# Kernel optimization log

Hardware: AMD Instinct MI355X
Metric: run time of the kernel (lower is better)

The kernel has to match this reference:

```python
import jax, jax.numpy as jnp
import numpy as np

# ---- constants baked into the module (buffers / init defaults) ----
SAMPLE_RATE = 44100
K = 1.0 / SAMPLE_RATE                    # time step
MAX_OM = 10000.0 * 2.0 * np.pi           # fmax * 2*pi
MIN_OM = 20.0 * 2.0 * np.pi
LX = 0.5
TAU0, TAU1 = 6.0, 1.0
LOSS_F1 = 500.0
_OM2 = 2.0 * np.pi * LOSS_F1
_DOMSQ = _OM2 ** 2                        # OmDamp1 = 0
ALPHA = np.float32(3.0 * np.log(10.0) / _DOMSQ * (_OM2 ** 2 / TAU0))
BETA = np.float32(3.0 * np.log(10.0) / _DOMSQ * (1.0 / TAU1 - 1.0 / TAU0))
M_MAX = N_MAX = 80
_gm, _gn = np.meshgrid(np.arange(1, M_MAX + 1), np.arange(1, N_MAX + 1), indexing='ij')
M_VEC = jnp.asarray(_gm.reshape(-1), dtype=jnp.float32)   # [6400]
N_VEC = jnp.asarray(_gn.reshape(-1), dtype=jnp.float32)   # [6400]


def setup_inputs() -> dict:
    z = jnp.zeros((), dtype=jnp.float32)
    return {
        'mu_raw': z, 'D_over_mu_raw': z, 'T0_over_mu_raw': z,
        'Ly_raw': z, 'xo_raw': z, 'yo_raw': z,
        'num_samples': 44100,  # duration=1.0 s
    }


def reference(mu_raw, D_over_mu_raw, T0_over_mu_raw, Ly_raw, xo_raw, yo_raw, num_samples):
    sp = jax.nn.softplus
    mu = sp(mu_raw) + 1e-4
    D_over_mu = sp(D_over_mu_raw) + 1e-4
    T0_over_mu = sp(T0_over_mu_raw) + 1e-4
    Ly = 1.1 + (4.0 - 1.1) * ((jnp.tanh(Ly_raw) + 1.0) / 2.0)
    xo = 0.49 * LX + (1.0 - 0.49) * LX * ((jnp.tanh(xo_raw) + 1.0) / 2.0)
    yo = 0.51 * Ly + (1.0 - 0.51) * Ly * ((jnp.tanh(yo_raw) + 1.0) / 2.0)
    xi = 0.1 * LX
    yi = 0.1 * Ly

    pi = np.float32(np.pi)
    g1 = (M_VEC * pi / LX) ** 2 + (N_VEC * pi / Ly) ** 2          # [6400]
    omega = jnp.sqrt(jax.nn.relu(T0_over_mu * g1 + D_over_mu * g1 * g1))
    valid = ((omega <= MAX_OM) & (omega >= MIN_OM)).astype(omega.dtype)

    in_w = jnp.cos(xi * pi * M_VEC / LX) * jnp.cos(yi * pi * N_VEC / Ly)
    out_w = jnp.cos(xo * pi * M_VEC / LX) * jnp.cos(yo * pi * N_VEC / Ly)
    sigma = ALPHA + BETA * omega ** 2
    ms = 0.25 * mu * LX * Ly
    P = out_w * in_w * (K ** 2) * jnp.exp(-sigma * K) / ms * valid  # [6400]

    n = jnp.arange(num_samples, dtype=jnp.float32)                # [N]
    # [6400, N] damped-sinusoid matrix, then reduce over modes
    decay_env = jnp.exp(-sigma[:, None] * (n[None, :] - 1.0) * K)
    sine = jnp.sin(n[None, :] * (omega[:, None] * K)) / (jnp.sin(omega * K) + 1e-8)[:, None]
    displacement = jnp.sum(P[:, None] * decay_env * sine, axis=0)  # [N]

    # normalize=True, velCalc=False (module defaults)
    peak = jnp.max(jnp.abs(displacement)) + 1e-8
    return displacement / peak
```

## Files before the change

### kernel.cpp

```cpp
#include <hip/hip_runtime.h>
#include <math.h>

#define BLK 256
#define G 32
#define NMODES 6400
#define STRIPE (NMODES / G)
#define MDIM 80
#define TILE 1024
#define SPT 4

__device__ float4   g_rec1[NMODES];
__device__ float4   g_rec2[NMODES];
__device__ unsigned g_maxbits;

__device__ __forceinline__ float v_fract(float x){ float r; asm("v_fract_f32 %0, %1" : "=v"(r) : "v"(x)); return r; }
__device__ __forceinline__ float v_sin_rev(float x){ float r; asm("v_sin_f32 %0, %1" : "=v"(r) : "v"(x)); return r; }
__device__ __forceinline__ float v_cos_rev(float x){ float r; asm("v_cos_f32 %0, %1" : "=v"(r) : "v"(x)); return r; }
__device__ __forceinline__ float v_exp2(float x){ float r; asm("v_exp_f32 %0, %1" : "=v"(r) : "v"(x)); return r; }

__device__ __forceinline__ double softplus_d(double x) {
    return (x > 30.0) ? x : log1p(exp(x));
}

__global__ __launch_bounds__(BLK) void setup_kernel(
    const float* __restrict__ mu_raw_p, const float* __restrict__ Dmu_raw_p,
    const float* __restrict__ T0mu_raw_p, const float* __restrict__ Ly_raw_p,
    const float* __restrict__ xo_raw_p, const float* __restrict__ yo_raw_p)
{
    const int gid = blockIdx.x * BLK + threadIdx.x;
    if (gid == 0) g_maxbits = 0u;
    if (gid >= NMODES) return;

    const double PI_D     = 3.14159265358979323846;
    const double TWO_PI_D = 6.28318530717958647693;
    const double INV2PI_D = 0.15915494309189533577;
    const double LOG2E_D  = 1.44269504088896340736;
    const double LX = 0.5;
    const double Kd = 1.0 / 44100.0;
    const double MAX_OM = 10000.0 * TWO_PI_D;
    const double MIN_OM = 20.0 * TWO_PI_D;

    const double OM2   = TWO_PI_D * 500.0;
    const double DOMSQ = OM2 * OM2;
    const float ALPHA_F = (float)(3.0 * log(10.0) / DOMSQ * (OM2 * OM2 / 6.0));
    const float BETA_F  = (float)(3.0 * log(10.0) / DOMSQ * (1.0 / 1.0 - 1.0 / 6.0));

    const double mu   = softplus_d((double)mu_raw_p[0])  + 1e-4;
    const double Dmu  = softplus_d((double)Dmu_raw_p[0]) + 1e-4;
    const double T0mu = softplus_d((double)T0mu_raw_p[0]) + 1e-4;
    const double Ly   = 1.1 + (4.0 - 1.1) * ((tanh((double)Ly_raw_p[0]) + 1.0) * 0.5);
    const double xo   = 0.49 * LX + (1.0 - 0.49) * LX * ((tanh((double)xo_raw_p[0]) + 1.0) * 0.5);
    const double yo   = 0.51 * Ly + (1.0 - 0.51) * Ly * ((tanh((double)yo_raw_p[0]) + 1.0) * 0.5);
    const double xi = 0.1 * LX;
    const double yi = 0.1 * Ly;
    const double ms = 0.25 * mu * LX * Ly;

    const double mm = (double)(gid / MDIM + 1);
    const double nn = (double)(gid % MDIM + 1);
    const double a1 = mm * PI_D / LX;
    const double a2 = nn * PI_D / Ly;
    const double g1 = a1 * a1 + a2 * a2;
    double osq = T0mu * g1 + Dmu * g1 * g1;
    if (osq < 0.0) osq = 0.0;
    const double omega = sqrt(osq);

    float4 r1 = make_float4(0.0f, 0.0f, 0.0f, 0.0f);
    float4 r2 = make_float4(1.0f, 0.0f, 1.0f, 0.0f);
    if (omega >= MIN_OM && omega <= MAX_OM) {
        const double w     = omega * Kd;
        const double sig   = (double)ALPHA_F + (double)BETA_F * (omega * omega);
        const double in_w  = cos(xi * a1) * cos(yi * a2);
        const double out_w = cos(xo * a1) * cos(yo * a2);
        const double denom = sin(w) + 1e-8;
        const double A = out_w * in_w * (Kd * Kd) / ms / denom;
        const double wrev = w * INV2PI_D;
        const float hi = (float)wrev;
        const float lo = (float)(wrev - (double)hi);
        const double z = -sig * Kd * LOG2E_D;
        const double dph = 256.0 * w;
        r1 = make_float4(hi, lo, (float)z, (float)A);
        r2 = make_float4((float)cos(dph), (float)sin(dph),
                         (float)exp2(256.0 * z), 0.0f);
    }
    g_rec1[gid] = r1;
    g_rec2[gid] = r2;
}

__global__ __launch_bounds__(BLK) void modal_main_kernel(
    float* __restrict__ partial, int pstride)
{
    __shared__ float4 md1[STRIPE];
    __shared__ float4 md2[STRIPE];
    __shared__ int cnt;
    if (threadIdx.x == 0) cnt = 0;
    __syncthreads();

    const int n0  = blockIdx.x * TILE;
    const int gy  = blockIdx.y;
    const float n0f = (float)n0;
    const int lane = threadIdx.x & 63;

    {
        const int j = threadIdx.x;
        bool alive = false;
        float4 o1, o2;
        if (j < STRIPE) {
            const float4 rec = g_rec1[gy + G * j];
            if (rec.w != 0.0f) {
                const float amp0 = rec.w * v_exp2(rec.z * n0f);
                if (fabsf(amp0) >= 1e-20f) {
                    const double wrev = (double)rec.x + (double)rec.y;
                    const double p0   = (double)n0 * wrev;
                    const float base  = (float)(p0 - rint(p0));
                    o1 = make_float4(base, rec.x, rec.z, amp0);
                    o2 = g_rec2[gy + G * j];
                    alive = true;
                }
            }
        }
        const unsigned long long mask = __ballot(alive);
        const int nw = __popcll(mask);
        int base_slot = 0;
        if (lane == 0 && nw) base_slot = atomicAdd(&cnt, nw);
        base_slot = __shfl(base_slot, 0, 64);
        if (alive) {
            const int s = base_slot + __popcll(mask & ((1ull << lane) - 1ull));
            md1[s] = o1;
            md2[s] = o2;
        }
    }
    __syncthreads();

    const int count = cnt;
    const float tf = (float)threadIdx.x;
    float acc0 = 0.0f, acc1 = 0.0f, acc2 = 0.0f, acc3 = 0.0f;
    for (int j = 0; j < count; ++j) {
        const float4 v1 = md1[j];
        const float4 v2 = md2[j];
        const float rev = v_fract(fmaf(tf, v1.y, v1.x));
        float s = v_sin_rev(rev);
        float c = v_cos_rev(rev);
        float amp = v1.w * v_exp2(v1.z * tf);
        acc0 = fmaf(amp, s, acc0);
        const float cD = v2.x, sD = v2.y, eD = v2.z;
        float s1 = fmaf(s, cD,  c * sD);
        float c1 = fmaf(c, cD, -s * sD);
        amp *= eD;
        acc1 = fmaf(amp, s1, acc1);
        float s2 = fmaf(s1, cD,  c1 * sD);
        float c2 = fmaf(c1, cD, -s1 * sD);
        amp *= eD;
        acc2 = fmaf(amp, s2, acc2);
        float s3 = fmaf(s2, cD,  c2 * sD);
        amp *= eD;
        acc3 = fmaf(amp, s3, acc3);
        (void)c2; (void)s3;
    }
    float* row = partial + (size_t)gy * pstride + n0 + threadIdx.x;
    row[0]   = acc0;
    row[256] = acc1;
    row[512] = acc2;
    row[768] = acc3;
}

__global__ __launch_bounds__(BLK) void combine_max_kernel(
    const float* __restrict__ partial, int pstride,
    float* __restrict__ out, int N)
{
    const int nvec = N >> 2;
    const int i = blockIdx.x * BLK + threadIdx.x;
    float m = 0.0f;
    if (i < nvec) {
        float4 s = make_float4(0.0f, 0.0f, 0.0f, 0.0f);
        const float4* p4 = (const float4*)partial;
        const int vstride = pstride >> 2;
        #pragma unroll
        for (int g = 0; g < G; ++g) {
            const float4 v = p4[(size_t)g * vstride + i];
            s.x += v.x; s.y += v.y; s.z += v.z; s.w += v.w;
        }
        ((float4*)out)[i] = s;
        m = fmaxf(fmaxf(fabsf(s.x), fabsf(s.y)), fmaxf(fabsf(s.z), fabsf(s.w)));
    }
    if (blockIdx.x == 0 && threadIdx.x < (N & 3)) {
        const int n = (nvec << 2) + threadIdx.x;
        float sv = 0.0f;
        for (int g = 0; g < G; ++g) sv += partial[(size_t)g * pstride + n];
        out[n] = sv;
        m = fmaxf(m, fabsf(sv));
    }
    #pragma unroll
    for (int o = 32; o > 0; o >>= 1) m = fmaxf(m, __shfl_down(m, o));
    __shared__ float sm[4];
    const int w = threadIdx.x >> 6, l = threadIdx.x & 63;
    if (l == 0) sm[w] = m;
    __syncthreads();
    if (threadIdx.x == 0) {
        const float mm = fmaxf(fmaxf(sm[0], sm[1]), fmaxf(sm[2], sm[3]));
        atomicMax(&g_maxbits, __float_as_uint(mm));
    }
}

__global__ __launch_bounds__(BLK) void scale_kernel(float* __restrict__ out, int N)
{
    const float inv = 1.0f / (__uint_as_float(g_maxbits) + 1e-8f);
    const int nvec = N >> 2;
    const int i = blockIdx.x * BLK + threadIdx.x;
    if (i < nvec) {
        float4 v = ((float4*)out)[i];
        v.x *= inv; v.y *= inv; v.z *= inv; v.w *= inv;
        ((float4*)out)[i] = v;
    }
    if (blockIdx.x == 0 && threadIdx.x < (N & 3))
        out[(nvec << 2) + threadIdx.x] *= inv;
}

extern "C" void kernel_launch(void* const* d_in, const int* in_sizes, int n_in,
                              void* d_out, int out_size, void* d_ws, size_t ws_size,
                              hipStream_t stream) {
    const float* mu_raw   = (const float*)d_in[0];
    const float* Dmu_raw  = (const float*)d_in[1];
    const float* T0mu_raw = (const float*)d_in[2];
    const float* Ly_raw   = (const float*)d_in[3];
    const float* xo_raw   = (const float*)d_in[4];
    const float* yo_raw   = (const float*)d_in[5];
    float* out = (float*)d_out;
    float* partial = (float*)d_ws;
    const int N = out_size;

    const int ntiles  = (N + TILE - 1) / TILE;
    const int pstride = ntiles * TILE;
    const int nb_setup = (NMODES + BLK - 1) / BLK;
    int nbv = ((N >> 2) + BLK - 1) / BLK;
    if (nbv < 1) nbv = 1;

    setup_kernel<<<nb_setup, BLK, 0, stream>>>(mu_raw, Dmu_raw, T0mu_raw,
                                               Ly_raw, xo_raw, yo_raw);
    modal_main_kernel<<<dim3(ntiles, G), BLK, 0, stream>>>(partial, pstride);
    combine_max_kernel<<<nbv, BLK, 0, stream>>>(partial, pstride, out, N);
    scale_kernel<<<nbv, BLK, 0, stream>>>(out, N);
}
```

Measured before the change: 92.35 us.

## Extend rotation recurrence to 8 samples, fuse combine with scale, transpose mode records

Doubles the time tile so each thread produces 8 samples per mode. Seven of them come from a cheap rotation recurrence, so the transcendental sin/cos/exp2 cost per output drops. Mode records are stored in stripe-contiguous order so the per-block staging loads coalesce, and the setup kernel uses 64-thread blocks. The separate combine and scale kernels become one kernel that uses an atomic spin-wait grid barrier to get the global peak, saving a launch and a reread of the output. The trade-offs are more error growth along the longer recurrence, half as many blocks in the main kernel, and a spin barrier that relies on all 44 blocks being co-resident.

```diff
diff --git a/kernel.cpp b/kernel.cpp
--- a/kernel.cpp
+++ b/kernel.cpp
@@ -2,16 +2,18 @@
 #include <math.h>
 
 #define BLK 256
+#define SBLK 64
 #define G 32
 #define NMODES 6400
 #define STRIPE (NMODES / G)
 #define MDIM 80
-#define TILE 1024
-#define SPT 4
+#define TILE 2048
+#define SPT 8
 
 __device__ float4   g_rec1[NMODES];
 __device__ float4   g_rec2[NMODES];
 __device__ unsigned g_maxbits;
+__device__ unsigned g_done;
 
 __device__ __forceinline__ float v_fract(float x){ float r; asm("v_fract_f32 %0, %1" : "=v"(r) : "v"(x)); return r; }
 __device__ __forceinline__ float v_sin_rev(float x){ float r; asm("v_sin_f32 %0, %1" : "=v"(r) : "v"(x)); return r; }
@@ -22,13 +24,13 @@
     return (x > 30.0) ? x : log1p(exp(x));
 }
 
-__global__ __launch_bounds__(BLK) void setup_kernel(
+__global__ __launch_bounds__(SBLK) void setup_kernel(
     const float* __restrict__ mu_raw_p, const float* __restrict__ Dmu_raw_p,
     const float* __restrict__ T0mu_raw_p, const float* __restrict__ Ly_raw_p,
     const float* __restrict__ xo_raw_p, const float* __restrict__ yo_raw_p)
 {
-    const int gid = blockIdx.x * BLK + threadIdx.x;
-    if (gid == 0) g_maxbits = 0u;
+    const int gid = blockIdx.x * SBLK + threadIdx.x;
+    if (gid == 0) { g_maxbits = 0u; g_done = 0u; }
     if (gid >= NMODES) return;
 
     const double PI_D     = 3.14159265358979323846;
@@ -82,8 +84,9 @@
         r2 = make_float4((float)cos(dph), (float)sin(dph),
                          (float)exp2(256.0 * z), 0.0f);
     }
-    g_rec1[gid] = r1;
-    g_rec2[gid] = r2;
+    const int slot = (gid % G) * STRIPE + (gid / G);
+    g_rec1[slot] = r1;
+    g_rec2[slot] = r2;
 }
 
 __global__ __launch_bounds__(BLK) void modal_main_kernel(
@@ -105,7 +108,7 @@
         bool alive = false;
         float4 o1, o2;
         if (j < STRIPE) {
-            const float4 rec = g_rec1[gy + G * j];
+            const float4 rec = g_rec1[gy * STRIPE + j];
             if (rec.w != 0.0f) {
                 const float amp0 = rec.w * v_exp2(rec.z * n0f);
                 if (fabsf(amp0) >= 1e-20f) {
@@ -113,7 +116,7 @@
                     const double p0   = (double)n0 * wrev;
                     const float base  = (float)(p0 - rint(p0));
                     o1 = make_float4(base, rec.x, rec.z, amp0);
-                    o2 = g_rec2[gy + G * j];
+                    o2 = g_rec2[gy * STRIPE + j];
                     alive = true;
                 }
             }
@@ -133,7 +136,10 @@
 
     const int count = cnt;
     const float tf = (float)threadIdx.x;
-    float acc0 = 0.0f, acc1 = 0.0f, acc2 = 0.0f, acc3 = 0.0f;
+    float acc[SPT];
+    #pragma unroll
+    for (int k = 0; k < SPT; ++k) acc[k] = 0.0f;
+
     for (int j = 0; j < count; ++j) {
         const float4 v1 = md1[j];
         const float4 v2 = md2[j];
@@ -141,37 +147,32 @@
         float s = v_sin_rev(rev);
         float c = v_cos_rev(rev);
         float amp = v1.w * v_exp2(v1.z * tf);
-        acc0 = fmaf(amp, s, acc0);
         const float cD = v2.x, sD = v2.y, eD = v2.z;
-        float s1 = fmaf(s, cD,  c * sD);
-        float c1 = fmaf(c, cD, -s * sD);
-        amp *= eD;
-        acc1 = fmaf(amp, s1, acc1);
-        float s2 = fmaf(s1, cD,  c1 * sD);
-        float c2 = fmaf(c1, cD, -s1 * sD);
-        amp *= eD;
-        acc2 = fmaf(amp, s2, acc2);
-        float s3 = fmaf(s2, cD,  c2 * sD);
-        amp *= eD;
-        acc3 = fmaf(amp, s3, acc3);
-        (void)c2; (void)s3;
+        acc[0] = fmaf(amp, s, acc[0]);
+        #pragma unroll
+        for (int k = 1; k < SPT; ++k) {
+            const float sn = fmaf(s, cD,  c * sD);
+            const float cn = fmaf(c, cD, -s * sD);
+            s = sn; c = cn;
+            amp *= eD;
+            acc[k] = fmaf(amp, s, acc[k]);
+        }
     }
     float* row = partial + (size_t)gy * pstride + n0 + threadIdx.x;
-    row[0]   = acc0;
-    row[256] = acc1;
-    row[512] = acc2;
-    row[768] = acc3;
-}
-
-__global__ __launch_bounds__(BLK) void combine_max_kernel(
+    #pragma unroll
+    for (int k = 0; k < SPT; ++k) row[k * 256] = acc[k];
+}
+
+__global__ __launch_bounds__(BLK) void combine_scale_kernel(
     const float* __restrict__ partial, int pstride,
-    float* __restrict__ out, int N)
+    float* __restrict__ out, int N, unsigned nblocks)
 {
     const int nvec = N >> 2;
     const int i = blockIdx.x * BLK + threadIdx.x;
+    float4 s = make_float4(0.0f, 0.0f, 0.0f, 0.0f);
     float m = 0.0f;
-    if (i < nvec) {
-        float4 s = make_float4(0.0f, 0.0f, 0.0f, 0.0f);
+    const bool has = (i < nvec);
+    if (has) {
         const float4* p4 = (const float4*)partial;
         const int vstride = pstride >> 2;
         #pragma unroll
@@ -179,40 +180,39 @@
             const float4 v = p4[(size_t)g * vstride + i];
             s.x += v.x; s.y += v.y; s.z += v.z; s.w += v.w;
         }
-        ((float4*)out)[i] = s;
         m = fmaxf(fmaxf(fabsf(s.x), fabsf(s.y)), fmaxf(fabsf(s.z), fabsf(s.w)));
     }
-    if (blockIdx.x == 0 && threadIdx.x < (N & 3)) {
+    float tail = 0.0f;
+    const bool has_tail = (blockIdx.x == 0 && threadIdx.x < (N & 3));
+    if (has_tail) {
         const int n = (nvec << 2) + threadIdx.x;
-        float sv = 0.0f;
-        for (int g = 0; g < G; ++g) sv += partial[(size_t)g * pstride + n];
-        out[n] = sv;
-        m = fmaxf(m, fabsf(sv));
+        for (int g = 0; g < G; ++g) tail += partial[(size_t)g * pstride + n];
+        m = fmaxf(m, fabsf(tail));
     }
     #pragma unroll
     for (int o = 32; o > 0; o >>= 1) m = fmaxf(m, __shfl_down(m, o));
     __shared__ float sm[4];
+    __shared__ float s_inv;
     const int w = threadIdx.x >> 6, l = threadIdx.x & 63;
     if (l == 0) sm[w] = m;
     __syncthreads();
     if (threadIdx.x == 0) {
-        const float mm = fmaxf(fmaxf(sm[0], sm[1]), fmaxf(sm[2], sm[3]));
-        atomicMax(&g_maxbits, __float_as_uint(mm));
-    }
-}
-
-__global__ __launch_bounds__(BLK) void scale_kernel(float* __restrict__ out, int N)
-{
-    const float inv = 1.0f / (__uint_as_float(g_maxbits) + 1e-8f);
-    const int nvec = N >> 2;
-    const int i = blockIdx.x * BLK + threadIdx.x;
-    if (i < nvec) {
-        float4 v = ((float4*)out)[i];
-        v.x *= inv; v.y *= inv; v.z *= inv; v.w *= inv;
-        ((float4*)out)[i] = v;
-    }
-    if (blockIdx.x == 0 && threadIdx.x < (N & 3))
-        out[(nvec << 2) + threadIdx.x] *= inv;
+        const float bm = fmaxf(fmaxf(sm[0], sm[1]), fmaxf(sm[2], sm[3]));
+        atomicMax(&g_maxbits, __float_as_uint(bm));
+        __threadfence();
+        atomicAdd(&g_done, 1u);
+        while (atomicAdd(&g_done, 0u) < nblocks) {}
+        __threadfence();
+        const float peak = __uint_as_float(atomicMax(&g_maxbits, 0u));
+        s_inv = 1.0f / (peak + 1e-8f);
+    }
+    __syncthreads();
+    const float inv = s_inv;
+    if (has) {
+        s.x *= inv; s.y *= inv; s.z *= inv; s.w *= inv;
+        ((float4*)out)[i] = s;
+    }
+    if (has_tail) out[(nvec << 2) + threadIdx.x] = tail * inv;
 }
 
 extern "C" void kernel_launch(void* const* d_in, const int* in_sizes, int n_in,
@@ -230,13 +230,13 @@
 
     const int ntiles  = (N + TILE - 1) / TILE;
     const int pstride = ntiles * TILE;
-    const int nb_setup = (NMODES + BLK - 1) / BLK;
+    const int nb_setup = (NMODES + SBLK - 1) / SBLK;
     int nbv = ((N >> 2) + BLK - 1) / BLK;
     if (nbv < 1) nbv = 1;
 
-    setup_kernel<<<nb_setup, BLK, 0, stream>>>(mu_raw, Dmu_raw, T0mu_raw,
-                                               Ly_raw, xo_raw, yo_raw);
+    setup_kernel<<<nb_setup, SBLK, 0, stream>>>(mu_raw, Dmu_raw, T0mu_raw,
+                                                Ly_raw, xo_raw, yo_raw);
     modal_main_kernel<<<dim3(ntiles, G), BLK, 0, stream>>>(partial, pstride);
-    combine_max_kernel<<<nbv, BLK, 0, stream>>>(partial, pstride, out, N);
-    scale_kernel<<<nbv, BLK, 0, stream>>>(out, N);
-}
+    combine_scale_kernel<<<nbv, BLK, 0, stream>>>(partial, pstride, out, N,
+                                                  (unsigned)nbv);
+}
```

After: 93.32 us. Within noise of the previous version (+1.1%).
